# Kernel optimization log

Measured on AMD Instinct MI355X. Metric: run time of the kernel, lower is better.

Reference implementation:

```python
import jax, jax.numpy as jnp
import numpy as np

VOCAB = 32000
BATCH = 256
SEQ = 2048


def setup_inputs() -> dict:
    key = jax.random.key(0)
    docs = jax.random.randint(key, (BATCH, SEQ), 0, VOCAB)  # int32 token ids
    return {"docs": docs}


def reference(docs):
    # Equivalent to mean(one_hot(docs, VOCAB), axis=-2) but computed as a
    # normalized histogram via scatter-add -- never materializes the
    # [B, S, V] one-hot tensor.
    B, S = docs.shape
    rows = jnp.arange(B)[:, None]  # [B, 1] broadcast against [B, S] tokens
    hist = jnp.zeros((B, VOCAB), dtype=jnp.float32).at[rows, docs].add(1.0)
    return hist / jnp.float32(S)
```

## Files before the change

### kernel.cpp

```cpp
#include <hip/hip_runtime.h>


#define VOCAB 32000
#define BATCH 256
#define SEQ   2048
#define NCHUNK 4
#define CHUNK (VOCAB / NCHUNK)
#define BLK   256

__global__ __launch_bounds__(BLK) void bow_hist_kernel(
    const int* __restrict__ docs, float* __restrict__ out) {
    __shared__ unsigned int bins[CHUNK];

    const int wg   = blockIdx.x;
    const int b    = wg >> 2;
    const int c    = wg & (NCHUNK - 1);
    const int base = c * CHUNK;
    const int tid  = threadIdx.x;

    #pragma unroll
    for (int i = tid; i < CHUNK; i += BLK) bins[i] = 0u;
    __syncthreads();

    const int4* row4 = reinterpret_cast<const int4*>(docs + (size_t)b * SEQ);
    #pragma unroll
    for (int it = 0; it < SEQ / 4 / BLK; ++it) {
        int4 t = row4[it * BLK + tid];
        int r0 = t.x - base, r1 = t.y - base, r2 = t.z - base, r3 = t.w - base;
        if ((unsigned)r0 < (unsigned)CHUNK) atomicAdd(&bins[r0], 1u);
        if ((unsigned)r1 < (unsigned)CHUNK) atomicAdd(&bins[r1], 1u);
        if ((unsigned)r2 < (unsigned)CHUNK) atomicAdd(&bins[r2], 1u);
        if ((unsigned)r3 < (unsigned)CHUNK) atomicAdd(&bins[r3], 1u);
    }
    __syncthreads();

    float* orow = out + (size_t)b * VOCAB + base;
    const float inv = 1.0f / (float)SEQ;
    #pragma unroll
    for (int i = tid; i < CHUNK / 4; i += BLK) {
        float4 v;
        v.x = (float)bins[i * 4 + 0] * inv;
        v.y = (float)bins[i * 4 + 1] * inv;
        v.z = (float)bins[i * 4 + 2] * inv;
        v.w = (float)bins[i * 4 + 3] * inv;
        reinterpret_cast<float4*>(orow)[i] = v;
    }
}

extern "C" void kernel_launch(void* const* d_in, const int* in_sizes, int n_in,
                              void* d_out, int out_size, void* d_ws, size_t ws_size,
                              hipStream_t stream) {
    const int* docs = (const int*)d_in[0];
    float* out = (float*)d_out;
    dim3 grid(BATCH * NCHUNK);
    dim3 block(BLK);
    bow_hist_kernel<<<grid, block, 0, stream>>>(docs, out);
}
```

Baseline: 13.06 us.

## Split vocab into eight chunks, prefetch tokens before zeroing, vectorize LDS access

Doubles the number of vocab chunks per batch row, which halves the LDS histogram per workgroup and doubles the grid size for more occupancy. Token loads are issued before the shared-memory zeroing so global latency overlaps the clear. LDS zeroing and readback now use 128-bit accesses. In exchange, each row of tokens is read from global memory twice as many times, and each workgroup checks every token against a smaller range.

```diff
diff --git a/kernel.cpp b/kernel.cpp
--- a/kernel.cpp
+++ b/kernel.cpp
@@ -4,7 +4,7 @@
 #define VOCAB 32000
 #define BATCH 256
 #define SEQ   2048
-#define NCHUNK 4
+#define NCHUNK 8
 #define CHUNK (VOCAB / NCHUNK)
 #define BLK   256
 
@@ -13,36 +13,43 @@
     __shared__ unsigned int bins[CHUNK];
 
     const int wg   = blockIdx.x;
-    const int b    = wg >> 2;
+    const int b    = wg >> 3;
     const int c    = wg & (NCHUNK - 1);
     const int base = c * CHUNK;
     const int tid  = threadIdx.x;
 
+    const int4* row4 = reinterpret_cast<const int4*>(docs + (size_t)b * SEQ);
+    int4 t0 = row4[tid];
+    int4 t1 = row4[BLK + tid];
+
+    uint4* bins4 = reinterpret_cast<uint4*>(bins);
     #pragma unroll
-    for (int i = tid; i < CHUNK; i += BLK) bins[i] = 0u;
+    for (int i = tid; i < CHUNK / 4; i += BLK) {
+        bins4[i] = make_uint4(0u, 0u, 0u, 0u);
+    }
     __syncthreads();
 
-    const int4* row4 = reinterpret_cast<const int4*>(docs + (size_t)b * SEQ);
-    #pragma unroll
-    for (int it = 0; it < SEQ / 4 / BLK; ++it) {
-        int4 t = row4[it * BLK + tid];
-        int r0 = t.x - base, r1 = t.y - base, r2 = t.z - base, r3 = t.w - base;
-        if ((unsigned)r0 < (unsigned)CHUNK) atomicAdd(&bins[r0], 1u);
-        if ((unsigned)r1 < (unsigned)CHUNK) atomicAdd(&bins[r1], 1u);
-        if ((unsigned)r2 < (unsigned)CHUNK) atomicAdd(&bins[r2], 1u);
-        if ((unsigned)r3 < (unsigned)CHUNK) atomicAdd(&bins[r3], 1u);
-    }
+    int r;
+    r = t0.x - base; if ((unsigned)r < (unsigned)CHUNK) atomicAdd(&bins[r], 1u);
+    r = t0.y - base; if ((unsigned)r < (unsigned)CHUNK) atomicAdd(&bins[r], 1u);
+    r = t0.z - base; if ((unsigned)r < (unsigned)CHUNK) atomicAdd(&bins[r], 1u);
+    r = t0.w - base; if ((unsigned)r < (unsigned)CHUNK) atomicAdd(&bins[r], 1u);
+    r = t1.x - base; if ((unsigned)r < (unsigned)CHUNK) atomicAdd(&bins[r], 1u);
+    r = t1.y - base; if ((unsigned)r < (unsigned)CHUNK) atomicAdd(&bins[r], 1u);
+    r = t1.z - base; if ((unsigned)r < (unsigned)CHUNK) atomicAdd(&bins[r], 1u);
+    r = t1.w - base; if ((unsigned)r < (unsigned)CHUNK) atomicAdd(&bins[r], 1u);
     __syncthreads();
 
     float* orow = out + (size_t)b * VOCAB + base;
     const float inv = 1.0f / (float)SEQ;
     #pragma unroll
     for (int i = tid; i < CHUNK / 4; i += BLK) {
+        uint4 u = bins4[i];
         float4 v;
-        v.x = (float)bins[i * 4 + 0] * inv;
-        v.y = (float)bins[i * 4 + 1] * inv;
-        v.z = (float)bins[i * 4 + 2] * inv;
-        v.w = (float)bins[i * 4 + 3] * inv;
+        v.x = (float)u.x * inv;
+        v.y = (float)u.y * inv;
+        v.z = (float)u.z * inv;
+        v.w = (float)u.w * inv;
         reinterpret_cast<float4*>(orow)[i] = v;
     }
 }
```

Result: slower. 18.32 us (+40.3%).
